# Kernel tuning notes

Measured on AMD Instinct MI355X. Metric: run time of the kernel, lower is better.

## Reference

```python
import jax, jax.numpy as jnp
import numpy as np

N, E, F = 32768, 524288, 16          # nodes, edges, num_filters
S_IN, V_IN = 64, 32                  # input irreps: 64x0e + 32x1o  (dim 64 + 96 = 160)
NRBF = 32                            # radial basis size of f_ij
LN2 = float(np.log(2.0))

def ssp(x):
    # shifted softplus, the standard SchNet activation
    return jax.nn.softplus(x) - LN2

def setup_inputs() -> dict:
    key = jax.random.key(0)
    ks = jax.random.split(key, 16)
    x = jax.random.normal(ks[0], (N, S_IN + 3 * V_IN), jnp.float32)
    idx_i = jax.random.randint(ks[1], (E,), 0, N)
    idx_j = jax.random.randint(ks[2], (E,), 0, N)
    f_ij = jax.random.normal(ks[3], (E, NRBF), jnp.float32)
    rcut_ij = jax.random.uniform(ks[4], (E,), jnp.float32)
    Yr_ij = jax.random.normal(ks[5], (E, 4), jnp.float32)  # 1x0e + 1x1o
    # equivariant Linear 1: (64x0e+32x1o) -> num_filters*(1x0e+1x1o) = 16x0e+16x1o
    W1_0e = jax.random.normal(ks[6], (S_IN, F), jnp.float32)
    W1_1o = jax.random.normal(ks[7], (V_IN, F), jnp.float32)
    # filter MLP: NRBF -> F -> num_irreps(6*F)
    mW1 = jax.random.normal(ks[8], (NRBF, F), jnp.float32) / np.sqrt(NRBF)
    mb1 = jnp.zeros((F,), jnp.float32)
    mW2 = jax.random.normal(ks[9], (F, 6 * F), jnp.float32) / np.sqrt(F)
    mb2 = jnp.zeros((6 * F,), jnp.float32)
    # equivariant Linear 2: (2Fx0e+2Fx1o+Fx1e+Fx2e) -> input irreps (1e/2e paths drop)
    W2_0e = jax.random.normal(ks[10], (2 * F, S_IN), jnp.float32)
    W2_1o = jax.random.normal(ks[11], (2 * F, V_IN), jnp.float32)
    # equivariant Linear 3: input irreps -> input irreps
    W3_0e = jax.random.normal(ks[12], (S_IN, S_IN), jnp.float32)
    W3_1o = jax.random.normal(ks[13], (V_IN, V_IN), jnp.float32)
    return dict(x=x, f_ij=f_ij, rcut_ij=rcut_ij, Yr_ij=Yr_ij,
                W1_0e=W1_0e, W1_1o=W1_1o, mW1=mW1, mb1=mb1, mW2=mW2, mb2=mb2,
                W2_0e=W2_0e, W2_1o=W2_1o, W3_0e=W3_0e, W3_1o=W3_1o,
                idx_i=idx_i, idx_j=idx_j)

def reference(x, f_ij, rcut_ij, Yr_ij, W1_0e, W1_1o, mW1, mb1, mW2, mb2,
              W2_0e, W2_1o, W3_0e, W3_1o, idx_i, idx_j):
    n = x.shape[0]
    s = x[:, :S_IN]                                  # [N, 64]  0e channels
    v = x[:, S_IN:].reshape(n, V_IN, 3)              # [N, 32, 3] 1o channels
    # Linear 1 (per-irrep channel mixing, e3nn fan-in normalization)
    s1 = (s @ W1_0e) / np.sqrt(S_IN)                 # [N, F]
    v1 = jnp.einsum('ncd,cf->nfd', v, W1_1o) / np.sqrt(V_IN)  # [N, F, 3]
    # gather neighbor features (x_j = x[idx_j], mul_to_axis -> per-filter irreps)
    sj = s1[idx_j]                                   # [E, F]
    vj = v1[idx_j]                                   # [E, F, 3]
    y0 = Yr_ij[:, 0]                                 # [E]
    y1 = Yr_ij[:, 1:4]                               # [E, 3]
    # tensor product (0e+1o) x (0e+1o) -> 2x0e + 2x1o + 1x1e + 1x2e, per filter
    o0a = sj * y0[:, None]                                            # 0e: 0e x 0e
    o0b = jnp.einsum('efd,ed->ef', vj, y1) / np.sqrt(3.0)             # 0e: 1o.1o
    o1a = sj[:, :, None] * y1[:, None, :]                             # 1o: 0e x 1o
    o1b = vj * y0[:, None, None]                                      # 1o: 1o x 0e
    o1e = jnp.cross(vj, y1[:, None, :]) / np.sqrt(2.0)                # 1e: 1o ^ 1o
    ux, uy, uz = vj[..., 0], vj[..., 1], vj[..., 2]
    wx, wy, wz = y1[:, None, 0], y1[:, None, 1], y1[:, None, 2]
    o2 = jnp.stack([(ux * wy + uy * wx) / np.sqrt(2.0),
                    (uy * wz + uz * wy) / np.sqrt(2.0),
                    (2.0 * uz * wz - ux * wx - uy * wy) / np.sqrt(6.0),
                    (ux * wz + uz * wx) / np.sqrt(2.0),
                    (ux * wx - uy * wy) / np.sqrt(2.0)], axis=-1)      # 2e [E, F, 5]
    # filter MLP on radial features, gated by cutoff; one scalar per irrep
    W = ssp(f_ij @ mW1 + mb1) @ mW2 + mb2            # [E, 6F]
    W = W * rcut_ij[:, None]
    w0a, w0b, w1a, w1b, w1e, w2 = (W[:, k * F:(k + 1) * F] for k in range(6))
    seg = lambda z: jax.ops.segment_sum(z, idx_i, num_segments=N)
    # modulate + scatter-sum into center atoms
    n0a = seg(o0a * w0a); n0b = seg(o0b * w0b)                          # [N, F]
    n1a = seg(o1a * w1a[:, :, None]); n1b = seg(o1b * w1b[:, :, None])  # [N, F, 3]
    n1e = seg(o1e * w1e[:, :, None])                                    # [N, F, 3] (dropped by Linear 2)
    n2 = seg(o2 * w2[:, :, None])                                       # [N, F, 5] (dropped by Linear 2)
    n0 = jnp.concatenate([n0a, n0b], axis=-1)        # [N, 2F] 0e
    n1 = jnp.concatenate([n1a, n1b], axis=1)         # [N, 2F, 3] 1o
    del n1e, n2  # no matching output irrep in input_irreps -> e3nn Linear drops them
    # Linear 2 back to input irreps
    s2 = (n0 @ W2_0e) / np.sqrt(2 * F)               # [N, 64]
    v2 = jnp.einsum('nfd,fc->ncd', n1, W2_1o) / np.sqrt(2 * F)  # [N, 32, 3]
    # scalar activation on l=0 only
    s2 = ssp(s2)
    # Linear 3
    s3 = (s2 @ W3_0e) / np.sqrt(S_IN)
    v3 = jnp.einsum('ncd,ce->ned', v2, W3_1o) / np.sqrt(V_IN)
    return jnp.concatenate([s3, v3.reshape(n, -1)], axis=-1)  # [N, 160]
```

## Files before the change

kernel.cpp:

```cpp
#include <hip/hip_runtime.h>
#include <math.h>

#define NN 32768
#define NE 524288
#define RSTR 32

__device__ __forceinline__ float sspf(float x) {
    const float INVLN2 = 1.4426950408889634f;
    const float LN2    = 0.69314718055994530942f;
    float t = __builtin_amdgcn_exp2f(-fabsf(x) * INVLN2);
    return fmaxf(x, 0.0f) + LN2 * __builtin_amdgcn_logf(1.0f + t) - LN2;
}

__global__ __launch_bounds__(256) void hist_kernel(
    const int* __restrict__ idx_i, int* __restrict__ counts)
{
    int e = blockIdx.x * 256 + threadIdx.x;
    atomicAdd(&counts[idx_i[e]], 1);
}

__global__ __launch_bounds__(1024) void scan_kernel(
    const int* __restrict__ counts, int* __restrict__ start, int* __restrict__ cursor)
{
    __shared__ int tmp[1024];
    int tid = threadIdx.x;
    int base = tid * 32;
    int local[32];
    int sum = 0;
    const int4* c4 = (const int4*)(counts + base);
#pragma unroll
    for (int q = 0; q < 8; q++) {
        int4 v = c4[q];
        local[q*4+0] = sum; sum += v.x;
        local[q*4+1] = sum; sum += v.y;
        local[q*4+2] = sum; sum += v.z;
        local[q*4+3] = sum; sum += v.w;
    }
    tmp[tid] = sum;
    __syncthreads();
    for (int off = 1; off < 1024; off <<= 1) {
        int v = 0;
        if (tid >= off) v = tmp[tid - off];
        __syncthreads();
        if (tid >= off) tmp[tid] += v;
        __syncthreads();
    }
    int excl = tmp[tid] - sum;
#pragma unroll
    for (int k = 0; k < 32; k++) {
        int s = excl + local[k];
        start[base + k] = s;
        cursor[base + k] = s;
    }
    if (tid == 1023) start[NN] = tmp[1023];
}

__global__ __launch_bounds__(256) void pack_kernel(
    const float* __restrict__ f_ij,
    const float* __restrict__ rcut_ij,
    const float* __restrict__ Yr,
    const int*   __restrict__ idx_i,
    const int*   __restrict__ idx_j,
    const float* __restrict__ mW1,
    const float* __restrict__ mb1,
    int* __restrict__ cursor,
    float* __restrict__ epack)
{
    __shared__ float sW1[512];
    __shared__ float sb1[16];
    int t = threadIdx.x;
    for (int k = t; k < 512; k += 256) sW1[k] = mW1[k];
    if (t < 16) sb1[t] = mb1[t];
    __syncthreads();

    int e = blockIdx.x * 256 + t;
    float h[16];
#pragma unroll
    for (int f = 0; f < 16; f++) h[f] = sb1[f];
    const float4* frow = (const float4*)(f_ij + (size_t)e * 32);
#pragma unroll
    for (int rq = 0; rq < 8; rq++) {
        float4 fv = frow[rq];
        int r = rq * 4;
#pragma unroll
        for (int f = 0; f < 16; f++)
            h[f] += fv.x * sW1[(r+0)*16+f] + fv.y * sW1[(r+1)*16+f]
                  + fv.z * sW1[(r+2)*16+f] + fv.w * sW1[(r+3)*16+f];
    }
    float rc = rcut_ij[e];
#pragma unroll
    for (int f = 0; f < 16; f++) h[f] = sspf(h[f]) * rc;

    int i = idx_i[e];
    int j = idx_j[e];
    float4 y = ((const float4*)Yr)[e];
    int slot = atomicAdd(&cursor[i], 1);

    float* rec = epack + (size_t)slot * RSTR;
    float4* r4 = (float4*)rec;
#pragma unroll
    for (int q = 0; q < 4; q++) r4[q] = ((float4*)h)[q];
    r4[4] = y;
    float4 tail; tail.x = rc; tail.y = __int_as_float(j); tail.z = 0.f; tail.w = 0.f;
    r4[5] = tail;
    float4 z; z.x = 0.f; z.y = 0.f; z.z = 0.f; z.w = 0.f;
    r4[6] = z;
    r4[7] = z;
}

__global__ __launch_bounds__(256) void embed_kernel(
    const float* __restrict__ x,
    const float* __restrict__ W1s,
    const float* __restrict__ W1v,
    float* __restrict__ embed)
{
    __shared__ float sWs[1024];
    __shared__ float sWv[512];
    int t = threadIdx.x;
    for (int k = t; k < 1024; k += 256) sWs[k] = W1s[k];
    for (int k = t; k < 512;  k += 256) sWv[k] = W1v[k];
    __syncthreads();

    int n = blockIdx.x * 256 + t;
    const float* xr = x + (size_t)n * 160;

    float s1[16];
#pragma unroll
    for (int f = 0; f < 16; f++) s1[f] = 0.f;
#pragma unroll
    for (int cq = 0; cq < 16; cq++) {
        float4 sv = ((const float4*)xr)[cq];
        int c = cq * 4;
#pragma unroll
        for (int f = 0; f < 16; f++) {
            s1[f] += sv.x * sWs[(c+0)*16+f] + sv.y * sWs[(c+1)*16+f]
                   + sv.z * sWs[(c+2)*16+f] + sv.w * sWs[(c+3)*16+f];
        }
    }

    float v1[48];
#pragma unroll
    for (int k = 0; k < 48; k++) v1[k] = 0.f;
#pragma unroll
    for (int q = 0; q < 24; q++) {
        float4 vv = ((const float4*)(xr + 64))[q];
        float vals[4] = {vv.x, vv.y, vv.z, vv.w};
#pragma unroll
        for (int u = 0; u < 4; u++) {
            int m = q * 4 + u;
            int c = m / 3, d = m % 3;
            float val = vals[u];
#pragma unroll
            for (int f = 0; f < 16; f++)
                v1[f*3+d] += val * sWv[c*16+f];
        }
    }

    float ob[64];
    const float is32 = 0.17677669529663688f;
#pragma unroll
    for (int f = 0; f < 16; f++) {
        ob[f]      = s1[f] * 0.125f;
        ob[16 + f] = v1[f*3+0] * is32;
        ob[32 + f] = v1[f*3+1] * is32;
        ob[48 + f] = v1[f*3+2] * is32;
    }

    float4* eo = (float4*)(embed + (size_t)n * 64);
#pragma unroll
    for (int q = 0; q < 16; q++) eo[q] = ((float4*)ob)[q];
}

__global__ __launch_bounds__(256) void nodeagg_kernel(
    const float* __restrict__ embed,
    const float* __restrict__ epack,
    const int*   __restrict__ start,
    const float* __restrict__ mW2,
    const float* __restrict__ mb2,
    float* __restrict__ acc)
{
    __shared__ float sW2[1024];
    int t = threadIdx.x;
    for (int k = t; k < 1024; k += 256)
        sW2[k] = mW2[(k >> 6) * 96 + (k & 63)];
    __syncthreads();

    int gid = blockIdx.x * 256 + t;
    int node = gid >> 4;
    int f = gid & 15;

    float wga[16], wgb[16], wgc[16], wgd[16];
#pragma unroll
    for (int k = 0; k < 16; k++) {
        wga[k] = sW2[k*64 + f];
        wgb[k] = sW2[k*64 + 16 + f];
        wgc[k] = sW2[k*64 + 32 + f];
        wgd[k] = sW2[k*64 + 48 + f];
    }
    float b0a = mb2[f], b0b = mb2[16+f], b1a = mb2[32+f], b1b = mb2[48+f];

    float aa = 0.f, ab = 0.f;
    float A1a0 = 0.f, A1a1 = 0.f, A1a2 = 0.f;
    float A1b0 = 0.f, A1b1 = 0.f, A1b2 = 0.f;

    int s0 = start[node];
    int s1 = start[node+1];

    for (int q = s0; q < s1; q++) {
        const float* rec = epack + (size_t)q * RSTR;
        const float4* r4 = (const float4*)rec;
        float4 h0 = r4[0], h1 = r4[1], h2 = r4[2], h3 = r4[3];
        float4 y  = r4[4];
        float rc  = rec[20];
        int j = __float_as_int(rec[21]);

        const float* em = embed + (size_t)j * 64;
        float sj = em[f];
        float vx = em[16 + f];
        float vy = em[32 + f];
        float vz = em[48 + f];

        float w0a = rc*b0a, w0b = rc*b0b, w1a = rc*b1a, w1b = rc*b1b;
        float h[16] = {h0.x,h0.y,h0.z,h0.w, h1.x,h1.y,h1.z,h1.w,
                       h2.x,h2.y,h2.z,h2.w, h3.x,h3.y,h3.z,h3.w};
#pragma unroll
        for (int k = 0; k < 16; k++) {
            w0a += h[k] * wga[k];
            w0b += h[k] * wgb[k];
            w1a += h[k] * wgc[k];
            w1b += h[k] * wgd[k];
        }

        aa += sj * y.x * w0a;
        ab += (vx*y.y + vy*y.z + vz*y.w) * w0b;
        float sw = sj * w1a;
        A1a0 += sw * y.y;
        A1a1 += sw * y.z;
        A1a2 += sw * y.w;
        float yw = y.x * w1b;
        A1b0 += vx * yw;
        A1b1 += vy * yw;
        A1b2 += vz * yw;
    }

    const float is3 = 0.5773502691896258f;
    float* o = acc + (size_t)node * 128;
    o[f]       = aa;
    o[16 + f]  = ab * is3;
    o[32 + f]  = A1a0;
    o[48 + f]  = A1a1;
    o[64 + f]  = A1a2;
    o[80 + f]  = A1b0;
    o[96 + f]  = A1b1;
    o[112 + f] = A1b2;
}


__device__ __forceinline__ void v2_seg32(const float* a, int d, int cb,
    const float* __restrict__ W2v, float* V2, int ln)
{
    cb = __builtin_amdgcn_readfirstlane(cb);
    const float is32 = 0.17677669529663688f;
    float na[16], nb[16];
    const float4* pa = (const float4*)(a + 32 + 16*d);
    const float4* pb = (const float4*)(a + 80 + 16*d);
#pragma unroll
    for (int q = 0; q < 4; q++) { ((float4*)na)[q] = pa[q]; ((float4*)nb)[q] = pb[q]; }
    float tacc[32];
#pragma unroll
    for (int c = 0; c < 32; c++) tacc[c] = 0.f;
#pragma unroll
    for (int f = 0; f < 16; f++) {
        float fa = na[f], fb = nb[f];
#pragma unroll
        for (int c = 0; c < 32; c++)
            tacc[c] += fa * W2v[f*32 + cb + c] + fb * W2v[(16+f)*32 + cb + c];
    }
    float* row = V2 + (d*64 + ln) * 33 + cb;
#pragma unroll
    for (int c = 0; c < 32; c++) row[c] = tacc[c] * is32;
}

__device__ __forceinline__ void v2_seg16(const float* a, int d, int cb,
    const float* __restrict__ W2v, float* V2, int ln)
{
    cb = __builtin_amdgcn_readfirstlane(cb);
    const float is32 = 0.17677669529663688f;
    float na[16], nb[16];
    const float4* pa = (const float4*)(a + 32 + 16*d);
    const float4* pb = (const float4*)(a + 80 + 16*d);
#pragma unroll
    for (int q = 0; q < 4; q++) { ((float4*)na)[q] = pa[q]; ((float4*)nb)[q] = pb[q]; }
    float tacc[16];
#pragma unroll
    for (int c = 0; c < 16; c++) tacc[c] = 0.f;
#pragma unroll
    for (int f = 0; f < 16; f++) {
        float fa = na[f], fb = nb[f];
#pragma unroll
        for (int c = 0; c < 16; c++)
            tacc[c] += fa * W2v[f*32 + cb + c] + fb * W2v[(16+f)*32 + cb + c];
    }
    float* row = V2 + (d*64 + ln) * 33 + cb;
#pragma unroll
    for (int c = 0; c < 16; c++) row[c] = tacc[c] * is32;
}

__device__ __forceinline__ void v3_seg32(float* o, int d, int cb,
    const float* __restrict__ W3v, const float* V2, int ln)
{
    cb = __builtin_amdgcn_readfirstlane(cb);
    const float is32 = 0.17677669529663688f;
    float tacc[32];
#pragma unroll
    for (int c = 0; c < 32; c++) tacc[c] = 0.f;
    const float* row = V2 + (d*64 + ln) * 33;
#pragma unroll
    for (int k = 0; k < 32; k++) {
        float vk = row[k];
#pragma unroll
        for (int c = 0; c < 32; c++) tacc[c] += vk * W3v[k*32 + cb + c];
    }
#pragma unroll
    for (int c = 0; c < 32; c++) o[64 + (cb+c)*3 + d] = tacc[c] * is32;
}

__device__ __forceinline__ void v3_seg16(float* o, int d, int cb,
    const float* __restrict__ W3v, const float* V2, int ln)
{
    cb = __builtin_amdgcn_readfirstlane(cb);
    const float is32 = 0.17677669529663688f;
    float tacc[16];
#pragma unroll
    for (int c = 0; c < 16; c++) tacc[c] = 0.f;
    const float* row = V2 + (d*64 + ln) * 33;
#pragma unroll
    for (int k = 0; k < 32; k++) {
        float vk = row[k];
#pragma unroll
        for (int c = 0; c < 16; c++) tacc[c] += vk * W3v[k*32 + cb + c];
    }
#pragma unroll
    for (int c = 0; c < 16; c++) o[64 + (cb+c)*3 + d] = tacc[c] * is32;
}

__global__ __launch_bounds__(256) void out_kernel(
    const float* __restrict__ acc,
    const float* __restrict__ W2s,
    const float* __restrict__ W2v,
    const float* __restrict__ W3s,
    const float* __restrict__ W3v,
    float* __restrict__ out)
{
    __shared__ float S2[64*65];
    __shared__ float V2[3*64*33];
    int t = threadIdx.x;
    int w = t >> 6, ln = t & 63;
    int node = blockIdx.x * 64 + ln;
    const float* a = acc + (size_t)node * 128;
    float* o = out + (size_t)node * 160;
    const float is32 = 0.17677669529663688f;

    if (w < 2) {
        int cb = __builtin_amdgcn_readfirstlane(w * 32);
        float n0r[32];
#pragma unroll
        for (int q = 0; q < 8; q++) ((float4*)n0r)[q] = ((const float4*)a)[q];
        float tacc[32];
#pragma unroll
        for (int c = 0; c < 32; c++) tacc[c] = 0.f;
#pragma unroll
        for (int k = 0; k < 32; k++) {
            float nk = n0r[k];
#pragma unroll
            for (int c = 0; c < 32; c++) tacc[c] += nk * W2s[k*64 + cb + c];
        }
        float* row = S2 + ln*65 + cb;
#pragma unroll
        for (int c = 0; c < 32; c++) row[c] = sspf(tacc[c] * is32);
    } else if (w == 2) {
        v2_seg32(a, 0, 0,  W2v, V2, ln);
        v2_seg16(a, 1, 0,  W2v, V2, ln);
    } else {
        v2_seg16(a, 1, 16, W2v, V2, ln);
        v2_seg32(a, 2, 0,  W2v, V2, ln);
    }
    __syncthreads();
    if (w < 2) {
        int cb = __builtin_amdgcn_readfirstlane(w * 32);
        float tacc[32];
#pragma unroll
        for (int c = 0; c < 32; c++) tacc[c] = 0.f;
        const float* row = S2 + ln*65;
#pragma unroll
        for (int k = 0; k < 64; k++) {
            float sk = row[k];
#pragma unroll
            for (int c = 0; c < 32; c++) tacc[c] += sk * W3s[k*64 + cb + c];
        }
#pragma unroll
        for (int q = 0; q < 8; q++) {
            float4 r = {tacc[q*4+0]*0.125f, tacc[q*4+1]*0.125f,
                        tacc[q*4+2]*0.125f, tacc[q*4+3]*0.125f};
            ((float4*)(o + cb))[q] = r;
        }
    } else if (w == 2) {
        v3_seg32(o, 0, 0,  W3v, V2, ln);
        v3_seg16(o, 1, 0,  W3v, V2, ln);
    } else {
        v3_seg16(o, 1, 16, W3v, V2, ln);
        v3_seg32(o, 2, 0,  W3v, V2, ln);
    }
}

extern "C" void kernel_launch(void* const* d_in, const int* in_sizes, int n_in,
                              void* d_out, int out_size, void* d_ws, size_t ws_size,
                              hipStream_t stream) {
    const float* x     = (const float*)d_in[0];
    const float* f_ij  = (const float*)d_in[1];
    const float* rcut  = (const float*)d_in[2];
    const float* Yr    = (const float*)d_in[3];
    const float* W1s   = (const float*)d_in[4];
    const float* W1v   = (const float*)d_in[5];
    const float* mW1   = (const float*)d_in[6];
    const float* mb1   = (const float*)d_in[7];
    const float* mW2   = (const float*)d_in[8];
    const float* mb2   = (const float*)d_in[9];
    const float* W2s   = (const float*)d_in[10];
    const float* W2v   = (const float*)d_in[11];
    const float* W3s   = (const float*)d_in[12];
    const float* W3v   = (const float*)d_in[13];
    const int*   idx_i = (const int*)d_in[14];
    const int*   idx_j = (const int*)d_in[15];
    float* out = (float*)d_out;

    float* fws   = (float*)d_ws;
    float* embed = fws;
    float* acc   = embed + (size_t)NN * 64;
    float* epack = acc   + (size_t)NN * 128;
    int* ibase   = (int*)(epack + (size_t)NE * RSTR);
    int* counts  = ibase;
    int* start   = counts + NN;
    int* cursor  = start + NN + 1;

    hipMemsetAsync(counts, 0, (size_t)NN * sizeof(int), stream);
    hist_kernel<<<NE/256, 256, 0, stream>>>(idx_i, counts);
    scan_kernel<<<1, 1024, 0, stream>>>(counts, start, cursor);
    pack_kernel<<<NE/256, 256, 0, stream>>>(f_ij, rcut, Yr, idx_i, idx_j,
                                            mW1, mb1, cursor, epack);
    embed_kernel<<<NN/256, 256, 0, stream>>>(x, W1s, W1v, embed);
    nodeagg_kernel<<<(NN*16)/256, 256, 0, stream>>>(embed, epack, start, mW2, mb2, acc);
    out_kernel<<<NN/64, 256, 0, stream>>>(acc, W2s, W2v, W3s, W3v, out);
}
```

Baseline: 359.6 us.

## Precompute per-edge rank in histogram and stage packed records through LDS

The histogram kernel now records each edge's rank within its destination node, so the pack kernel computes its slot as start[i]+rank[e] and no longer needs a second atomic pass on a cursor array. Pack records are first written to shared memory, then written out cooperatively so that 8 lanes store one 128-byte record as consecutive float4s, replacing per-thread strided 128-byte stores. This trades an extra rank array write/read and LDS traffic plus a barrier for fewer global atomics and more coalesced scattered writes. Edge order within a node segment is still set by atomic order, so it stays nondeterministic.

```diff
diff --git a/kernel.cpp b/kernel.cpp
--- a/kernel.cpp
+++ b/kernel.cpp
@@ -4,6 +4,7 @@
 #define NN 32768
 #define NE 524288
 #define RSTR 32
+#define SREC_STR 36
 
 __device__ __forceinline__ float sspf(float x) {
     const float INVLN2 = 1.4426950408889634f;
@@ -13,14 +14,14 @@
 }
 
 __global__ __launch_bounds__(256) void hist_kernel(
-    const int* __restrict__ idx_i, int* __restrict__ counts)
+    const int* __restrict__ idx_i, int* __restrict__ counts, int* __restrict__ rank)
 {
     int e = blockIdx.x * 256 + threadIdx.x;
-    atomicAdd(&counts[idx_i[e]], 1);
+    rank[e] = atomicAdd(&counts[idx_i[e]], 1);
 }
 
 __global__ __launch_bounds__(1024) void scan_kernel(
-    const int* __restrict__ counts, int* __restrict__ start, int* __restrict__ cursor)
+    const int* __restrict__ counts, int* __restrict__ start)
 {
     __shared__ int tmp[1024];
     int tid = threadIdx.x;
@@ -48,9 +49,7 @@
     int excl = tmp[tid] - sum;
 #pragma unroll
     for (int k = 0; k < 32; k++) {
-        int s = excl + local[k];
-        start[base + k] = s;
-        cursor[base + k] = s;
+        start[base + k] = excl + local[k];
     }
     if (tid == 1023) start[NN] = tmp[1023];
 }
@@ -63,11 +62,14 @@
     const int*   __restrict__ idx_j,
     const float* __restrict__ mW1,
     const float* __restrict__ mb1,
-    int* __restrict__ cursor,
+    const int*   __restrict__ start,
+    const int*   __restrict__ rank,
     float* __restrict__ epack)
 {
     __shared__ float sW1[512];
     __shared__ float sb1[16];
+    __shared__ float srec[256 * SREC_STR];
+    __shared__ int   sslot[256];
     int t = threadIdx.x;
     for (int k = t; k < 512; k += 256) sW1[k] = mW1[k];
     if (t < 16) sb1[t] = mb1[t];
@@ -94,18 +96,31 @@
     int i = idx_i[e];
     int j = idx_j[e];
     float4 y = ((const float4*)Yr)[e];
-    int slot = atomicAdd(&cursor[i], 1);
-
-    float* rec = epack + (size_t)slot * RSTR;
-    float4* r4 = (float4*)rec;
-#pragma unroll
-    for (int q = 0; q < 4; q++) r4[q] = ((float4*)h)[q];
-    r4[4] = y;
+    int slot = start[i] + rank[e];
+
+    float* rp = srec + t * SREC_STR;
+    float4* rp4 = (float4*)rp;
+#pragma unroll
+    for (int q = 0; q < 4; q++) rp4[q] = ((float4*)h)[q];
+    rp4[4] = y;
     float4 tail; tail.x = rc; tail.y = __int_as_float(j); tail.z = 0.f; tail.w = 0.f;
-    r4[5] = tail;
+    rp4[5] = tail;
     float4 z; z.x = 0.f; z.y = 0.f; z.z = 0.f; z.w = 0.f;
-    r4[6] = z;
-    r4[7] = z;
+    rp4[6] = z;
+    rp4[7] = z;
+    sslot[t] = slot;
+    __syncthreads();
+
+    int lane = t & 63;
+    int wbase = t & 192;
+    int qi = lane & 7;
+#pragma unroll
+    for (int g = 0; g < 8; g++) {
+        int r = wbase + g * 8 + (lane >> 3);
+        int s = sslot[r];
+        float4 v = ((const float4*)(srec + r * SREC_STR))[qi];
+        ((float4*)(epack + (size_t)s * RSTR))[qi] = v;
+    }
 }
 
 __global__ __launch_bounds__(256) void embed_kernel(
@@ -441,13 +456,13 @@
     int* ibase   = (int*)(epack + (size_t)NE * RSTR);
     int* counts  = ibase;
     int* start   = counts + NN;
-    int* cursor  = start + NN + 1;
+    int* rank    = start + NN + 1;
 
     hipMemsetAsync(counts, 0, (size_t)NN * sizeof(int), stream);
-    hist_kernel<<<NE/256, 256, 0, stream>>>(idx_i, counts);
-    scan_kernel<<<1, 1024, 0, stream>>>(counts, start, cursor);
+    hist_kernel<<<NE/256, 256, 0, stream>>>(idx_i, counts, rank);
+    scan_kernel<<<1, 1024, 0, stream>>>(counts, start);
     pack_kernel<<<NE/256, 256, 0, stream>>>(f_ij, rcut, Yr, idx_i, idx_j,
-                                            mW1, mb1, cursor, epack);
+                                            mW1, mb1, start, rank, epack);
     embed_kernel<<<NN/256, 256, 0, stream>>>(x, W1s, W1v, embed);
     nodeagg_kernel<<<(NN*16)/256, 256, 0, stream>>>(embed, epack, start, mW2, mb2, acc);
     out_kernel<<<NN/64, 256, 0, stream>>>(acc, W2s, W2v, W3s, W3v, out);
```

Result: faster. 338.0 us (-6.0%).
